# Optimization experiments

Measured on AMD Instinct MI355X. Metric: run time of the kernel, lower is better.

The kernel has to match this reference:

```python
import jax, jax.numpy as jnp
import numpy as np
import math

B, S, SIG, EMB, LAT, H, L_ENC, L_DEC = 16, 1024, 256, 256, 256, 8, 2, 2
EH, DH = EMB // H, LAT // H
EPS = 1e-10


def _sinusoidal_last_row(d):
    # last row of a standard sinusoidal PE table (position index = max_len-1)
    pos = 5000.0 - 1.0
    i = np.arange(d)
    angles = pos / np.power(10000.0, (2 * (i // 2)) / d)
    pe = np.where(i % 2 == 0, np.sin(angles), np.cos(angles))
    return jnp.asarray(pe, dtype=jnp.float32)


def setup_inputs() -> dict:
    key = jax.random.key(0)
    ks = iter(jax.random.split(key, 64))
    w = lambda *sh: 0.05 * jax.random.normal(next(ks), sh, dtype=jnp.float32)
    z = lambda *sh: jnp.zeros(sh, dtype=jnp.float32)
    d = {
        'inputData': jax.random.normal(next(ks), (B, S, SIG), dtype=jnp.float32),
        'pos_enc': _sinusoidal_last_row(SIG),
        'embW': w(SIG, EMB), 'embb': z(EMB),
        'qW': w(EMB, EMB), 'qb': z(EMB),
        'kW': w(EMB, EMB), 'kb': z(EMB),
        'vW': w(EMB, EMB), 'vb': z(EMB),
        'encBW': w(EH, EH), 'encBb': z(EH),
        'oW': w(EMB, EMB), 'ob': z(EMB),
        'ffe_W1': w(EMB, 2 * EMB), 'ffe_b1': z(2 * EMB),
        'ffe_W2': w(2 * EMB, EMB), 'ffe_b2': z(EMB),
        'lnSA_g': jnp.ones((L_ENC, EMB)), 'lnSA_b': z(L_ENC, EMB),
        'lnFF_g': jnp.ones((L_ENC, EMB)), 'lnFF_b': z(L_ENC, EMB),
        'start': w(1, LAT),
        'decQW': w(LAT, LAT), 'decQb': z(LAT),
        'decKW': w(EMB, EMB), 'decKb': z(EMB),
        'decVW': w(EMB, LAT), 'decVb': z(LAT),
        'decBW': w(EH + DH, DH), 'decBb': z(DH),
        'latW': w(LAT, LAT), 'latb': z(LAT),
        'ffd_W1': w(LAT, LAT // 2), 'ffd_b1': z(LAT // 2),
        'ffd_W2': w(LAT // 2, LAT), 'ffd_b2': z(LAT),
        'lnCA_g': jnp.ones((L_DEC, LAT)), 'lnCA_b': z(L_DEC, LAT),
        'lnLFF_g': jnp.ones((L_DEC, LAT)), 'lnLFF_b': z(L_DEC, LAT),
        'finW': w(LAT, LAT), 'finb': z(LAT),
    }
    return d


def _ln(x, g, b):
    m = x.mean(-1, keepdims=True)
    v = x.var(-1, keepdims=True)
    return (x - m) * jax.lax.rsqrt(v + EPS) * g + b


def _enc_attn(x, qW, qb, kW, kb, vW, vb, bW, bb, oW, ob):
    # x: (B,S,EMB) -> heads (B,H,S,EH)
    sp = lambda t: t.reshape(B, S, H, EH).transpose(0, 2, 1, 3)
    q, k, v = sp(x @ qW + qb), sp(x @ kW + kb), sp(x @ vW + vb)
    bk = k @ bW + bb                                   # bilinear key (B,H,S,EH)
    attn = jax.nn.softmax(jnp.einsum('bhqd,bhkd->bhqk', q, bk) / math.sqrt(EH), axis=-1)
    out = jnp.einsum('bhqk,bhkd->bhqd', attn, v)
    out = out.transpose(0, 2, 1, 3).reshape(B, S, EMB)
    return out @ oW + ob


def _dec_attn(enc, lat, qW, qb, kW, kb, vW, vb, bW, bb, oW, ob):
    # lat: (B,LAT) single query token; enc: (B,S,EMB)
    q = (lat @ qW + qb).reshape(B, 1, H, DH).transpose(0, 2, 1, 3)   # (B,H,1,DH)
    k = (enc @ kW + kb).reshape(B, S, H, EH).transpose(0, 2, 1, 3)   # (B,H,S,EH)
    v = (enc @ vW + vb).reshape(B, S, H, DH).transpose(0, 2, 1, 3)   # (B,H,S,DH)
    qcat = jnp.broadcast_to(q, (B, H, S, DH))
    kcat = jnp.concatenate([k, qcat], axis=-1)                       # (B,H,S,EH+DH)
    bk = kcat @ bW + bb                                              # (B,H,S,DH)
    attn = jax.nn.softmax(jnp.einsum('bhqd,bhkd->bhqk', q, bk) / math.sqrt(EH + DH), axis=-1)
    out = jnp.einsum('bhqk,bhkd->bhqd', attn, v)                     # (B,H,1,DH)
    out = out.transpose(0, 2, 1, 3).reshape(B, LAT)
    return out @ oW + ob


def reference(inputData, pos_enc, embW, embb, qW, qb, kW, kb, vW, vb, encBW, encBb,
              oW, ob, ffe_W1, ffe_b1, ffe_W2, ffe_b2, lnSA_g, lnSA_b, lnFF_g, lnFF_b,
              start, decQW, decQb, decKW, decKb, decVW, decVb, decBW, decBb,
              latW, latb, ffd_W1, ffd_b1, ffd_W2, ffd_b2, lnCA_g, lnCA_b,
              lnLFF_g, lnLFF_b, finW, finb):
    emb = (inputData + pos_enc) @ embW + embb          # (B,S,EMB)
    t = emb
    for l in range(L_ENC):
        n = _ln(t, lnSA_g[l], lnSA_b[l])
        a = _enc_attn(n, qW, qb, kW, kb, vW, vb, encBW, encBb, oW, ob) + n
        t = a + emb
        n2 = _ln(t, lnFF_g[l], lnFF_b[l])
        ff = jax.nn.selu(n2 @ ffe_W1 + ffe_b1) @ ffe_W2 + ffe_b2
        t = ff + n2
    init_lat = jnp.broadcast_to(start, (B, LAT))
    lat = init_lat
    for l in range(L_DEC):
        nl = _ln(init_lat, lnCA_g[l], lnCA_b[l])       # module always feeds initialLatentData
        lat = _dec_attn(t, nl, decQW, decQb, decKW, decKb, decVW, decVb,
                        decBW, decBb, latW, latb)
        nf = _ln(lat, lnLFF_g[l], lnLFF_b[l])
        lat = jax.nn.selu(nf @ ffd_W1 + ffd_b1) @ ffd_W2 + ffd_b2
    return lat @ finW + finb
```

## Files before the change

### kernel.cpp

```cpp
#include <hip/hip_runtime.h>
#include <hip/hip_bf16.h>
#include <math.h>

typedef __hip_bfloat16 bf16;

#define BB 16
#define SS 1024
#define NH 8
#define NR (BB*SS)
#define SZE ((size_t)NR*256)
#define RS 264

typedef __attribute__((ext_vector_type(8))) short short8;
typedef __attribute__((ext_vector_type(4))) float f32x4;
typedef __attribute__((ext_vector_type(8))) unsigned short u16x8;
typedef __attribute__((ext_vector_type(4))) unsigned short u16x4;

__device__ __forceinline__ float bf2f(bf16 x){ return __bfloat162float(x); }
__device__ __forceinline__ bf16  f2bf(float x){ return __float2bfloat16(x); }
__device__ __forceinline__ unsigned short f2bfu(float x){
  bf16 t = __float2bfloat16(x); return *reinterpret_cast<unsigned short*>(&t);
}
__device__ __forceinline__ float bfu2f(unsigned short u){
  return __uint_as_float(((unsigned)u)<<16);
}

__device__ __forceinline__ void stT(float* p, size_t i, float v){ p[i] = v; }
__device__ __forceinline__ void stT(bf16*  p, size_t i, float v){ p[i] = f2bf(v); }

__device__ __forceinline__ float selu_f(float x){
  const float a = 1.6732632423543772f, sc = 1.0507009873554805f;
  return sc * (x > 0.f ? x : a * expm1f(x));
}

__device__ __forceinline__ void gload16(const void* g, void* l){
  __builtin_amdgcn_global_load_lds(
      (const __attribute__((address_space(1))) unsigned int*)g,
      (__attribute__((address_space(3))) unsigned int*)l, 16, 0, 0);
}

struct PtrPack { const void* p[43]; };
struct TabPack { int off[43]; int cnt[43]; int total; };
struct TrTab   { int srcOff[12]; int K[12]; int N[12]; int dstOff[12]; int total; };

__global__ __launch_bounds__(256) void k_canon(PtrPack ptrs, TabPack tab,
    float* __restrict__ dst, int* __restrict__ flagw)
{
  unsigned w0 = ((const unsigned*)ptrs.p[18])[0];
  int isbf = (w0 == 0x3F803F80u) ? 1 : 0;
  if (blockIdx.x == 0 && threadIdx.x == 0) *flagw = isbf;
  __shared__ int so[43], sn[43];
  int tid = threadIdx.x;
  if (tid < 43){ so[tid] = tab.off[tid]; sn[tid] = tab.cnt[tid]; }
  __syncthreads();
  int g = blockIdx.x*256 + tid;
  if (g >= tab.total) return;
  int seg = 1;
  while (seg < 42 && g >= so[seg] + sn[seg]) seg++;
  int li = g - so[seg];
  float v = isbf ? bf2f(((const bf16*)ptrs.p[seg])[li])
                 : ((const float*)ptrs.p[seg])[li];
  dst[g] = v;
}

__global__ __launch_bounds__(256) void k_transW(const float* __restrict__ wt,
    TrTab tt, unsigned short* __restrict__ dst)
{
  int g = blockIdx.x*256 + threadIdx.x;
  if (g >= tt.total) return;
  int seg = 0;
  while (seg < 11 && g >= tt.dstOff[seg] + tt.K[seg]*tt.N[seg]) seg++;
  int li = g - tt.dstOff[seg];
  int K = tt.K[seg], N = tt.N[seg];
  int n = li / K, k = li - n*K;
  dst[g] = f2bfu(wt[tt.srcOff[seg] + (size_t)k*N + n]);
}

__global__ __launch_bounds__(256) void k_qfold(const float* __restrict__ wt,
    int qOff, int qbOff, int bwOff, unsigned short* __restrict__ qW2t,
    float* __restrict__ qbf)
{
  __shared__ float bw[32];
  int n = blockIdx.x, t = threadIdx.x;
  int h = n>>5, d = n&31;
  if (t < 32) bw[t] = wt[bwOff + d*32 + t];
  __syncthreads();
  float acc = 0.f;
  #pragma unroll 8
  for (int j = 0; j < 32; j++) acc += wt[qOff + (size_t)t*256 + h*32 + j]*bw[j];
  qW2t[(size_t)n*256 + t] = f2bfu(acc);
  if (t == 0){
    float a = 0.f;
    #pragma unroll 8
    for (int j = 0; j < 32; j++) a += wt[qbOff + h*32 + j]*bw[j];
    qbf[n] = a;
  }
}

template<int K, int LDA, int CT>
__device__ __forceinline__ void wave_gemmN(const unsigned short (*As)[LDA],
    const unsigned short* __restrict__ Wt, int n0, f32x4 acc[4][CT], int lane)
{
  int col = lane & 15, quad = lane >> 4;
  #pragma unroll
  for (int k0 = 0; k0 < K; k0 += 32){
    short8 a[4], b[CT];
    #pragma unroll
    for (int rt = 0; rt < 4; rt++)
      a[rt] = *(const short8*)(&As[rt*16 + col][k0 + quad*8]);
    #pragma unroll
    for (int ct = 0; ct < CT; ct++)
      b[ct] = *(const short8*)(&Wt[(size_t)(n0 + ct*16 + col)*K + k0 + quad*8]);
    #pragma unroll
    for (int rt = 0; rt < 4; rt++)
      #pragma unroll
      for (int ct = 0; ct < CT; ct++)
        acc[rt][ct] = __builtin_amdgcn_mfma_f32_16x16x32_bf16(a[rt], b[ct], acc[rt][ct], 0, 0, 0);
  }
}

template<int K, int LDA, int CT>
__device__ __forceinline__ void wave_gemmM32(const unsigned short (*As)[LDA],
    const unsigned short* __restrict__ Wt, int n0, f32x4 acc[2][CT], int lane)
{
  int col = lane & 15, quad = lane >> 4;
  #pragma unroll
  for (int k0 = 0; k0 < K; k0 += 32){
    short8 a[2], b[CT];
    #pragma unroll
    for (int rt = 0; rt < 2; rt++)
      a[rt] = *(const short8*)(&As[rt*16 + col][k0 + quad*8]);
    #pragma unroll
    for (int ct = 0; ct < CT; ct++)
      b[ct] = *(const short8*)(&Wt[(size_t)(n0 + ct*16 + col)*K + k0 + quad*8]);
    #pragma unroll
    for (int rt = 0; rt < 2; rt++)
      #pragma unroll
      for (int ct = 0; ct < CT; ct++)
        acc[rt][ct] = __builtin_amdgcn_mfma_f32_16x16x32_bf16(a[rt], b[ct], acc[rt][ct], 0, 0, 0);
  }
}

#define ZERO_ACC4(acc)  { _Pragma("unroll") for (int rt=0;rt<4;rt++){ _Pragma("unroll") for (int ct=0;ct<4;ct++) acc[rt][ct] = (f32x4){0.f,0.f,0.f,0.f}; } }
#define ZERO_ACC2(acc)  { _Pragma("unroll") for (int rt=0;rt<4;rt++){ _Pragma("unroll") for (int ct=0;ct<2;ct++) acc[rt][ct] = (f32x4){0.f,0.f,0.f,0.f}; } }
#define ZERO_ACC24(acc) { _Pragma("unroll") for (int rt=0;rt<2;rt++){ _Pragma("unroll") for (int ct=0;ct<4;ct++) acc[rt][ct] = (f32x4){0.f,0.f,0.f,0.f}; } }

#define EPI_BEGIN(e) { int rt = (e)>>4, ct = ((e)>>2)&3, r = (e)&3; \
    int lrow = rt*16 + quad*4 + r; int gcol0 = ct*16 + col; \
    float av = acc[rt][ct][r]; (void)lrow; (void)gcol0; (void)av;
#define EPI_END }

#define EPI32_BEGIN(e) { int rt = (e)>>4, ct = ((e)>>2)&3, r = (e)&3; \
    int lrow = rt*16 + quad*4 + r; int gcol0 = ct*16 + col; \
    float av = acc[rt][ct][r]; (void)lrow; (void)gcol0; (void)av;
#define EPI32_END }

template<int PRE, typename OT>
__global__ __launch_bounds__(256) void k_gemm_mfma(const void* __restrict__ A,
    const int* __restrict__ flagp, const float* __restrict__ pe,
    const unsigned short* __restrict__ Wt, const float* __restrict__ bias,
    OT* __restrict__ out)
{
  __shared__ __align__(16) unsigned short As[64][RS];
  int tid = threadIdx.x;
  int m = blockIdx.x & 255, nh = blockIdx.x >> 8;
  int row0 = m*64;
  if (PRE == 0){
    int f = *flagp;
    if (f){
      for (int jj = 0; jj < 8; jj++){
        int idx = tid + jj*256;
        int row = idx>>5, c8 = (idx&31)<<3;
        u16x8 xb = *(const u16x8*)((const unsigned short*)A
            + (size_t)(row0+row)*256 + c8);
        u16x8 o;
        #pragma unroll
        for (int i=0;i<8;i++) o[i] = f2bfu(bfu2f(xb[i]) + pe[c8+i]);
        *(u16x8*)(&As[row][c8]) = o;
      }
    } else {
      for (int jj = 0; jj < 16; jj++){
        int idx = tid + jj*256;
        int row = idx>>6, c4 = (idx&63)<<2;
        float4 x = *(const float4*)((const float*)A + (size_t)(row0+row)*256 + c4);
        u16x4 o;
        o[0] = f2bfu(x.x + pe[c4+0]);
        o[1] = f2bfu(x.y + pe[c4+1]);
        o[2] = f2bfu(x.z + pe[c4+2]);
        o[3] = f2bfu(x.w + pe[c4+3]);
        *(u16x4*)(&As[row][c4]) = o;
      }
    }
  } else {
    for (int jj = 0; jj < 16; jj++){
      int idx = tid + jj*256;
      int row = idx>>6, c4 = (idx&63)<<2;
      float4 x = *(const float4*)((const float*)A + (size_t)(row0+row)*256 + c4);
      *(u16x4*)(&As[row][c4]) = (u16x4){f2bfu(x.x),f2bfu(x.y),f2bfu(x.z),f2bfu(x.w)};
    }
  }
  __syncthreads();
  int w = tid>>6, lane = tid&63, col = lane&15, quad = lane>>4;
  int n0 = nh*128 + w*32;
  f32x4 acc[4][2];
  ZERO_ACC2(acc);
  wave_gemmN<256, RS, 2>(As, Wt, n0, acc, lane);
  #pragma unroll
  for (int rt = 0; rt < 4; rt++){
    #pragma unroll
    for (int ct = 0; ct < 2; ct++){
      #pragma unroll
      for (int r = 0; r < 4; r++){
        int grow = row0 + rt*16 + quad*4 + r;
        int gcol = n0 + ct*16 + col;
        stT(out, (size_t)grow*256 + gcol, acc[rt][ct][r] + bias[gcol]);
      }
    }
  }
}

__global__ __launch_bounds__(256) void k_decKV(const float* __restrict__ A,
    const unsigned short* __restrict__ KWt, const float* __restrict__ kb,
    const unsigned short* __restrict__ VWt, const float* __restrict__ vb,
    bf16* __restrict__ ko, bf16* __restrict__ vo)
{
  __shared__ __align__(16) unsigned short As[64][RS];
  int tid = threadIdx.x;
  int m = blockIdx.x & 255, nh = blockIdx.x >> 8;
  int row0 = m*64;
  for (int jj = 0; jj < 16; jj++){
    int idx = tid + jj*256;
    int row = idx>>6, c4 = (idx&63)<<2;
    float4 x = *(const float4*)(A + (size_t)(row0+row)*256 + c4);
    *(u16x4*)(&As[row][c4]) = (u16x4){f2bfu(x.x),f2bfu(x.y),f2bfu(x.z),f2bfu(x.w)};
  }
  __syncthreads();
  int w = tid>>6, lane = tid&63, col = lane&15, quad = lane>>4;
  int n0 = nh*128 + w*32;
  f32x4 acc[4][2];
  ZERO_ACC2(acc);
  wave_gemmN<256, RS, 2>(As, KWt, n0, acc, lane);
  #pragma unroll
  for (int rt = 0; rt < 4; rt++){
    #pragma unroll
    for (int ct = 0; ct < 2; ct++){
      #pragma unroll
      for (int r = 0; r < 4; r++){
        int grow = row0 + rt*16 + quad*4 + r;
        int gcol = n0 + ct*16 + col;
        ko[(size_t)grow*256 + gcol] = f2bf(acc[rt][ct][r] + kb[gcol]);
      }
    }
  }
  ZERO_ACC2(acc);
  wave_gemmN<256, RS, 2>(As, VWt, n0, acc, lane);
  #pragma unroll
  for (int rt = 0; rt < 4; rt++){
    #pragma unroll
    for (int ct = 0; ct < 2; ct++){
      #pragma unroll
      for (int r = 0; r < 4; r++){
        int grow = row0 + rt*16 + quad*4 + r;
        int gcol = n0 + ct*16 + col;
        vo[(size_t)grow*256 + gcol] = f2bf(acc[rt][ct][r] + vb[gcol]);
      }
    }
  }
}

__global__ __launch_bounds__(256) void k_qkvbk_mfma(const float* __restrict__ tsrc,
    const float* __restrict__ lng, const float* __restrict__ lnb,
    const unsigned short* __restrict__ qW2t, const float* __restrict__ qbf,
    const unsigned short* __restrict__ kWt, const float* __restrict__ kb,
    const unsigned short* __restrict__ vWt, const float* __restrict__ vb,
    bf16* __restrict__ qo, bf16* __restrict__ vo, bf16* __restrict__ bko)
{
  __shared__ __align__(16) unsigned short Ns[64][RS];
  __shared__ float mArr[64], rArr[64];
  int tid = threadIdx.x;
  int m = blockIdx.x & 255, nh = blockIdx.x >> 8;
  int row0 = m*64;
  int b = row0 >> 10, s0 = row0 & 1023;
  {
    int row = tid>>2, l4 = tid&3;
    const float4* rp = (const float4*)(tsrc + (size_t)(row0+row)*256) + l4*16;
    float s = 0.f, s2 = 0.f;
    #pragma unroll 4
    for (int c = 0; c < 16; c++){
      float4 x = rp[c];
      s += x.x + x.y + x.z + x.w;
      s2 += x.x*x.x + x.y*x.y + x.z*x.z + x.w*x.w;
    }
    s  += __shfl_down(s, 2, 4);  s  += __shfl_down(s, 1, 4);
    s2 += __shfl_down(s2, 2, 4); s2 += __shfl_down(s2, 1, 4);
    if (l4 == 0){
      float mn = s*(1.f/256.f);
      float v = s2*(1.f/256.f) - mn*mn;
      mArr[row] = mn; rArr[row] = rsqrtf(fmaxf(v,0.f) + 1e-10f);
    }
  }
  __syncthreads();
  for (int jj = 0; jj < 16; jj++){
    int idx = tid + jj*256;
    int row = idx>>6, c4 = (idx&63)<<2;
    float4 x = *(const float4*)(tsrc + (size_t)(row0+row)*256 + c4);
    float mn = mArr[row], rr = rArr[row];
    u16x4 o;
    o[0] = f2bfu((x.x - mn)*rr*lng[c4+0] + lnb[c4+0]);
    o[1] = f2bfu((x.y - mn)*rr*lng[c4+1] + lnb[c4+1]);
    o[2] = f2bfu((x.z - mn)*rr*lng[c4+2] + lnb[c4+2]);
    o[3] = f2bfu((x.w - mn)*rr*lng[c4+3] + lnb[c4+3]);
    *(u16x4*)(&Ns[row][c4]) = o;
  }
  __syncthreads();
  int w = tid>>6, lane = tid&63, col = lane&15, quad = lane>>4;
  int n0 = nh*128 + w*32;
  f32x4 acc[4][2];
  ZERO_ACC2(acc);
  wave_gemmN<256, RS, 2>(Ns, qW2t, n0, acc, lane);
  #pragma unroll
  for (int rt = 0; rt < 4; rt++){
    #pragma unroll
    for (int ct = 0; ct < 2; ct++){
      #pragma unroll
      for (int r = 0; r < 4; r++){
        int grow = row0 + rt*16 + quad*4 + r;
        int gcol = n0 + ct*16 + col;
        qo[(size_t)grow*256 + gcol] = f2bf(acc[rt][ct][r] + qbf[gcol]);
      }
    }
  }
  ZERO_ACC2(acc);
  wave_gemmN<256, RS, 2>(Ns, vWt, n0, acc, lane);
  #pragma unroll
  for (int rt = 0; rt < 4; rt++){
    #pragma unroll
    for (int ct = 0; ct < 2; ct++){
      #pragma unroll
      for (int r = 0; r < 4; r++){
        int grow = row0 + rt*16 + quad*4 + r;
        int gcol = n0 + ct*16 + col;
        vo[(size_t)grow*256 + gcol] = f2bf(acc[rt][ct][r] + vb[gcol]);
      }
    }
  }
  ZERO_ACC2(acc);
  wave_gemmN<256, RS, 2>(Ns, kWt, n0, acc, lane);
  int h = nh*4 + w;
  #pragma unroll
  for (int rt = 0; rt < 4; rt++){
    #pragma unroll
    for (int ct = 0; ct < 2; ct++){
      #pragma unroll
      for (int r = 0; r < 4; r++){
        int srow = s0 + rt*16 + quad*4 + r;
        int d = ct*16 + col;
        bko[(((size_t)(b*NH+h))*SS + srow)*32 + d] =
            f2bf(acc[rt][ct][r] + kb[h*32 + d]);
      }
    }
  }
}

__global__ __launch_bounds__(256) void k_attn_mfma(
    const bf16* __restrict__ q, const bf16* __restrict__ bk,
    const bf16* __restrict__ v, bf16* __restrict__ ao)
{
  int bi = blockIdx.x;
  int qq = bi >> 7, b = (bi >> 3) & 15, h = bi & 7;
  int tid = threadIdx.x;
  int w = tid>>6, lane = tid&63;
  int quad = lane>>4, col = lane&15;
  int q0 = qq*128 + w*32;

  __shared__ __align__(16) unsigned short Ks2b[2][64][32];
  __shared__ __align__(16) unsigned short Vt2b[2][32][76];

  const float scale2 = 0.17677669529663687f * 1.4426950408889634f;
  short8 aq[2];
  #pragma unroll
  for (int rt = 0; rt < 2; rt++){
    const unsigned short* gq = (const unsigned short*)q
        + ((size_t)(b*SS + q0 + rt*16 + col))*256 + h*32 + quad*8;
    u16x8 qv = *(const u16x8*)gq;
    #pragma unroll
    for (int i=0;i<8;i++) aq[rt][i] = (short)f2bfu(bfu2f(qv[i])*scale2);
  }

  float l_r[2] = {0.f, 0.f};
  f32x4 o[2][2];
  #pragma unroll
  for (int rt=0;rt<2;rt++)
    #pragma unroll
    for (int ct=0;ct<2;ct++) o[rt][ct] = (f32x4){0.f,0.f,0.f,0.f};

  int krow = tid>>2, ksl = tid&3;
  int kslw = ksl ^ ((krow>>1)&3);
  int vk0 = tid>>3, vdg = tid&7;
  int vk1 = vk0 + 32;
  int rsl = (quad ^ ((col>>1)&3))*8;

  const unsigned short* bkp = (const unsigned short*)bk + ((size_t)(b*NH+h))*SS*32;
  const unsigned short* vp  = (const unsigned short*)v + (size_t)b*SS*256 + h*32;

  u16x8 rK;
  u16x4 rV0, rV1;
  rK  = *(const u16x8*)(bkp + (size_t)krow*32 + ksl*8);
  rV0 = *(const u16x4*)(vp + (size_t)vk0*256 + vdg*4);
  rV1 = *(const u16x4*)(vp + (size_t)vk1*256 + vdg*4);

  for (int kt = 0; kt < 16; kt++){
    int cb = kt & 1;
    *(u16x8*)(&Ks2b[cb][krow][kslw*8]) = rK;
    #pragma unroll
    for (int i=0;i<4;i++) Vt2b[cb][vdg*4+i][vk0] = rV0[i];
    #pragma unroll
    for (int i=0;i<4;i++) Vt2b[cb][vdg*4+i][vk1] = rV1[i];
    __syncthreads();
    if (kt < 15){
      int nk = kt + 1;
      rK  = *(const u16x8*)(bkp + (size_t)(nk*64 + krow)*32 + ksl*8);
      rV0 = *(const u16x4*)(vp + (size_t)(nk*64 + vk0)*256 + vdg*4);
      rV1 = *(const u16x4*)(vp + (size_t)(nk*64 + vk1)*256 + vdg*4);
    }
    #pragma unroll
    for (int g = 0; g < 2; g++){
      unsigned pk[2][4];
      #pragma unroll
      for (int tt = 0; tt < 2; tt++){
        int t4 = g*2 + tt;
        short8 bk8 = *(const short8*)(&Ks2b[cb][t4*16 + col][rsl]);
        #pragma unroll
        for (int rt = 0; rt < 2; rt++){
          f32x4 s = __builtin_amdgcn_mfma_f32_16x16x32_bf16(bk8, aq[rt],
                      (f32x4){0.f,0.f,0.f,0.f}, 0, 0, 0);
          float e0 = __builtin_amdgcn_exp2f(s[0]);
          float e1 = __builtin_amdgcn_exp2f(s[1]);
          float e2 = __builtin_amdgcn_exp2f(s[2]);
          float e3 = __builtin_amdgcn_exp2f(s[3]);
          l_r[rt] += (e0+e1)+(e2+e3);
          pk[rt][tt*2+0] = __builtin_amdgcn_perm(
              __float_as_uint(e1), __float_as_uint(e0), 0x07060302u);
          pk[rt][tt*2+1] = __builtin_amdgcn_perm(
              __float_as_uint(e3), __float_as_uint(e2), 0x07060302u);
        }
      }
      short8 av[2];
      #pragma unroll
      for (int ct = 0; ct < 2; ct++){
        u16x4 v0 = *(const u16x4*)(&Vt2b[cb][ct*16+col][(g*2+0)*16 + quad*4]);
        u16x4 v1 = *(const u16x4*)(&Vt2b[cb][ct*16+col][(g*2+1)*16 + quad*4]);
        av[ct][0]=(short)v0[0]; av[ct][1]=(short)v0[1];
        av[ct][2]=(short)v0[2]; av[ct][3]=(short)v0[3];
        av[ct][4]=(short)v1[0]; av[ct][5]=(short)v1[1];
        av[ct][6]=(short)v1[2]; av[ct][7]=(short)v1[3];
      }
      #pragma unroll
      for (int rt = 0; rt < 2; rt++){
        union { unsigned u[4]; short8 s8; } pb;
        pb.u[0]=pk[rt][0]; pb.u[1]=pk[rt][1]; pb.u[2]=pk[rt][2]; pb.u[3]=pk[rt][3];
        #pragma unroll
        for (int ct = 0; ct < 2; ct++)
          o[rt][ct] = __builtin_amdgcn_mfma_f32_16x16x32_bf16(
              av[ct], pb.s8, o[rt][ct], 0, 0, 0);
      }
    }
  }
  #pragma unroll
  for (int rt=0;rt<2;rt++){
    float l = l_r[rt];
    l += __shfl_xor(l, 16, 64);
    l += __shfl_xor(l, 32, 64);
    float inv = 1.f / l;
    size_t obase = ((size_t)(b*SS + q0 + rt*16 + col))*256 + h*32;
    #pragma unroll
    for (int ct=0;ct<2;ct++){
      u16x4 ov;
      #pragma unroll
      for (int r=0;r<4;r++) ov[r] = f2bfu(o[rt][ct][r]*inv);
      *(u16x4*)((unsigned short*)ao + obase + ct*16 + quad*4) = ov;
    }
  }
}

__global__ __launch_bounds__(256) void k_oln_mfma(
    const float* __restrict__ tsrc, const float* __restrict__ emb,
    const bf16* __restrict__ ao,
    const float* __restrict__ lnSAg, const float* __restrict__ lnSAb,
    const unsigned short* __restrict__ oWt, const float* __restrict__ ob,
    const float* __restrict__ lnFFg, const float* __restrict__ lnFFb,
    bf16* __restrict__ n2o)
{
  __shared__ __align__(16) unsigned short Aos[32][RS];
  __shared__ __align__(16) unsigned short Tm[32][RS];
  __shared__ float mArr[32], rArr[32];
  int tid = threadIdx.x, row0 = blockIdx.x*32;
  {
    int row = tid>>3, l8 = tid&7;
    const float4* rp = (const float4*)(tsrc + (size_t)(row0+row)*256) + l8*8;
    float s = 0.f, s2 = 0.f;
    #pragma unroll
    for (int c = 0; c < 8; c++){
      float4 x = rp[c];
      s += x.x + x.y + x.z + x.w;
      s2 += x.x*x.x + x.y*x.y + x.z*x.z + x.w*x.w;
    }
    s  += __shfl_down(s, 4, 8);  s  += __shfl_down(s, 2, 8);  s  += __shfl_down(s, 1, 8);
    s2 += __shfl_down(s2, 4, 8); s2 += __shfl_down(s2, 2, 8); s2 += __shfl_down(s2, 1, 8);
    if (l8 == 0){
      float m = s*(1.f/256.f);
      float v = s2*(1.f/256.f) - m*m;
      mArr[row] = m; rArr[row] = rsqrtf(fmaxf(v,0.f) + 1e-10f);
    }
  }
  for (int jj = 0; jj < 4; jj++){
    int idx = tid + jj*256;
    int row = idx>>5, c8 = idx&31;
    *(u16x8*)(&Aos[row][c8*8]) =
        *(const u16x8*)((const unsigned short*)ao + (size_t)(row0+row)*256 + c8*8);
  }
  __syncthreads();
  int w = tid>>6, lane = tid&63, col = lane&15, quad = lane>>4;
  f32x4 acc[2][4];
  ZERO_ACC24(acc);
  wave_gemmM32<256, RS, 4>(Aos, oWt, w*64, acc, lane);
  #pragma unroll
  for (int e = 0; e < 32; e++){
    EPI32_BEGIN(e)
    int gcol = w*64 + gcol0;
    size_t g = (size_t)(row0+lrow)*256 + gcol;
    float n1 = (tsrc[g] - mArr[lrow])*rArr[lrow]*lnSAg[gcol] + lnSAb[gcol];
    Tm[lrow][gcol] = f2bfu(av + ob[gcol] + n1 + emb[g]);
    EPI32_END
  }
  __syncthreads();
  {
    int row = tid>>3, l8 = tid&7;
    float s = 0.f, s2 = 0.f;
    for (int c = l8; c < 256; c += 8){ float x = bfu2f(Tm[row][c]); s += x; s2 += x*x; }
    s  += __shfl_down(s, 4, 8);  s  += __shfl_down(s, 2, 8);  s  += __shfl_down(s, 1, 8);
    s2 += __shfl_down(s2, 4, 8); s2 += __shfl_down(s2, 2, 8); s2 += __shfl_down(s2, 1, 8);
    if (l8 == 0){
      float m = s*(1.f/256.f);
      float v = s2*(1.f/256.f) - m*m;
      mArr[row] = m; rArr[row] = rsqrtf(fmaxf(v,0.f) + 1e-10f);
    }
  }
  __syncthreads();
  for (int jj = 0; jj < 8; jj++){
    int idx = tid + jj*256;
    int row = idx>>6, c4 = (idx&63)<<2;
    float mn = mArr[row], rr = rArr[row];
    u16x4 tv = *(const u16x4*)(&Tm[row][c4]);
    u16x4 ov;
    ov[0] = f2bfu((bfu2f(tv[0]) - mn)*rr*lnFFg[c4+0] + lnFFb[c4+0]);
    ov[1] = f2bfu((bfu2f(tv[1]) - mn)*rr*lnFFg[c4+1] + lnFFb[c4+1]);
    ov[2] = f2bfu((bfu2f(tv[2]) - mn)*rr*lnFFg[c4+2] + lnFFb[c4+2]);
    ov[3] = f2bfu((bfu2f(tv[3]) - mn)*rr*lnFFg[c4+3] + lnFFb[c4+3]);
    *(u16x4*)((unsigned short*)n2o + (size_t)(row0+row)*256 + c4) = ov;
  }
}

#define FF_STAGE(B, KT) { \
  int k0 = (KT)*64; \
  _Pragma("unroll") \
  for (int i = 0; i < 4; i++){ int c = w*4 + i; \
    gload16(A  + (size_t)(row0 + c*8 + rsub)*KFULL + k0 + sgo, &As[B][c*512]); } \
  _Pragma("unroll") \
  for (int i = 0; i < 2; i++){ int c = w*2 + i; \
    gload16(Wb + (size_t)(n0   + c*8 + rsub)*KFULL + k0 + sgo, &Bs[B][c*512]); } }

#define FF_COMPUTE(B) { \
  _Pragma("unroll") \
  for (int kk = 0; kk < 2; kk++){ \
    short8 a[4], b2r[2]; \
    _Pragma("unroll") \
    for (int rt = 0; rt < 4; rt++) \
      a[rt] = *(const short8*)(&As[B][((wr*64 + rt*16 + col)<<6) + ((((kk<<2)|quad) ^ (col&7))<<3)]); \
    _Pragma("unroll") \
    for (int ct = 0; ct < 2; ct++) \
      b2r[ct] = *(const short8*)(&Bs[B][((wc*32 + ct*16 + col)<<6) + ((((kk<<2)|quad) ^ (col&7))<<3)]); \
    _Pragma("unroll") \
    for (int rt = 0; rt < 4; rt++) \
      _Pragma("unroll") \
      for (int ct = 0; ct < 2; ct++) \
        acc[rt][ct] = __builtin_amdgcn_mfma_f32_16x16x32_bf16(a[rt], b2r[ct], acc[rt][ct], 0, 0, 0); } }

template<int KFULL, int NFULL, int EPI>
__global__ __launch_bounds__(256) void k_ff_gemm(const bf16* __restrict__ A,
    const unsigned short* __restrict__ Wt, const float* __restrict__ bias,
    const bf16* __restrict__ res, void* __restrict__ outv)
{
  __shared__ __align__(16) unsigned short As[2][128*64];
  __shared__ __align__(16) unsigned short Bs[2][64*64];
  constexpr int NWG = 128 * (NFULL/64);
  constexpr int NKT = KFULL/64;
  int tid = threadIdx.x;
  int w = tid>>6, lane = tid&63;
  int col = lane&15, quad = lane>>4;
  int wr = w>>1, wc = w&1;
  int rsub = lane>>3;
  int sgo = (((lane&7) ^ rsub)<<3);
  int bid = blockIdx.x;
  int swz = (bid & 7)*(NWG>>3) + (bid >> 3);
  int mb = swz & 127, nb = swz >> 7;
  int row0 = mb*128, n0 = nb*64;
  const bf16* Wb = (const bf16*)Wt;

  f32x4 acc[4][2];
  ZERO_ACC2(acc);

  FF_STAGE(0, 0);
  __syncthreads();
  #pragma unroll
  for (int kt = 0; kt < NKT-1; kt++){
    int cb = kt & 1;
    FF_STAGE(cb^1, kt+1);
    FF_COMPUTE(cb);
    __syncthreads();
  }
  FF_COMPUTE((NKT-1)&1);

  if (EPI == 0){
    bf16* o = (bf16*)outv;
    #pragma unroll
    for (int rt = 0; rt < 4; rt++){
      #pragma unroll
      for (int ct = 0; ct < 2; ct++){
        #pragma unroll
        for (int r = 0; r < 4; r++){
          int grow = row0 + wr*64 + rt*16 + quad*4 + r;
          int gcol = n0 + wc*32 + ct*16 + col;
          o[(size_t)grow*NFULL + gcol] = f2bf(selu_f(acc[rt][ct][r] + bias[gcol]));
        }
      }
    }
  } else {
    float* o = (float*)outv;
    #pragma unroll
    for (int rt = 0; rt < 4; rt++){
      #pragma unroll
      for (int ct = 0; ct < 2; ct++){
        #pragma unroll
        for (int r = 0; r < 4; r++){
          int grow = row0 + wr*64 + rt*16 + quad*4 + r;
          int gcol = n0 + wc*32 + ct*16 + col;
          size_t g = (size_t)grow*NFULL + gcol;
          o[g] = acc[rt][ct][r] + bias[gcol] + bf2f(res[g]);
        }
      }
    }
  }
}

__global__ __launch_bounds__(256) void k_dec_head(const float* __restrict__ startp,
    const float* __restrict__ lng, const float* __restrict__ lnb,
    const float* __restrict__ decQW, const float* __restrict__ decQb,
    const float* __restrict__ decBW,
    float* __restrict__ s_q, float* __restrict__ s_qc)
{
  __shared__ float s1[256], s2[256], nl[256], qv[256];
  int t = threadIdx.x;
  float v = startp[t];
  s1[t]=v; s2[t]=v*v; __syncthreads();
  for (int s=128;s>0;s>>=1){
    if (t<s){ s1[t]+=s1[t+s]; s2[t]+=s2[t+s]; }
    __syncthreads();
  }
  float m = s1[0]*(1.f/256.f);
  float var = s2[0]*(1.f/256.f) - m*m;
  float r = rsqrtf(fmaxf(var,0.f) + 1e-10f);
  nl[t] = (v-m)*r*lng[t] + lnb[t];
  __syncthreads();
  float acc = decQb[t];
  for (int k=0;k<256;k++) acc += nl[k]*decQW[k*256+t];
  qv[t] = acc; s_q[t] = acc;
  __syncthreads();
  int h = t>>5, d = t&31;
  float a = 0.f;
  #pragma unroll 8
  for (int e=0;e<32;e++) a += qv[h*32+e]*decBW[(32+e)*32 + d];
  s_qc[t] = a;
}

__global__ __launch_bounds__(256) void k_bkdec_mfma(const bf16* __restrict__ kk,
    const float* __restrict__ qc, const unsigned short* __restrict__ decBWt,
    const float* __restrict__ Bb, bf16* __restrict__ bko)
{
  __shared__ __align__(16) unsigned short Ks[64][RS];
  int tid = threadIdx.x, row0 = blockIdx.x*64;
  int b = row0 >> 10, s0 = row0 & 1023;
  for (int jj = 0; jj < 8; jj++){
    int idx = tid + jj*256;
    int row = idx>>5, c8 = idx&31;
    *(u16x8*)(&Ks[row][c8*8]) =
        *(const u16x8*)((const unsigned short*)kk + (size_t)(row0+row)*256 + c8*8);
  }
  __syncthreads();
  int w = tid>>6, lane = tid&63, col = lane&15, quad = lane>>4;
  f32x4 acc[4][4];
  ZERO_ACC4(acc);
  #pragma unroll
  for (int ct = 0; ct < 4; ct++){
    int base = w*64 + ct*16;
    int h = base >> 5, d0 = base & 31;
    short8 bfrag = *(const short8*)(&decBWt[(size_t)(d0 + col)*32 + quad*8]);
    #pragma unroll
    for (int rt = 0; rt < 4; rt++){
      short8 afrag = *(const short8*)(&Ks[rt*16 + col][h*32 + quad*8]);
      acc[rt][ct] = __builtin_amdgcn_mfma_f32_16x16x32_bf16(afrag, bfrag, acc[rt][ct], 0, 0, 0);
    }
  }
  #pragma unroll
  for (int e = 0; e < 64; e++){
    EPI_BEGIN(e)
    int srow = s0 + lrow;
    int gcol = w*64 + gcol0;
    int h = gcol >> 5, d = gcol & 31;
    bko[(((size_t)(b*NH+h))*SS + srow)*32 + d] = f2bf(av + qc[gcol] + Bb[d]);
    EPI_END
  }
}

__global__ __launch_bounds__(256) void k_attn_dec(const float* __restrict__ q,
    const bf16* __restrict__ bk, const bf16* __restrict__ v,
    float* __restrict__ out)
{
  int h = blockIdx.x & 7, b = blockIdx.x >> 3;
  int tid = threadIdx.x;
  __shared__ float qs[32];
  __shared__ float sc[SS];
  __shared__ float red[256];
  if (tid < 32) qs[tid] = q[h*32 + tid] * (0.125f * 1.4426950408889634f);
  __syncthreads();
  float lsum = 0.f;
  for (int jj=0;jj<4;jj++){
    int j = tid*4 + jj;
    size_t base = (((size_t)(b*NH+h))*SS + j)*32;
    float s = 0.f;
    #pragma unroll
    for (int d=0;d<32;d++) s += qs[d]*bf2f(bk[base + d]);
    float e = __builtin_amdgcn_exp2f(s);
    sc[j] = e; lsum += e;
  }
  red[tid] = lsum; __syncthreads();
  for (int s=128;s>0;s>>=1){ if (tid<s) red[tid]+=red[tid+s]; __syncthreads(); }
  float gs = red[0];
  __syncthreads();
  int d = tid & 31, c = tid >> 5;
  float acc = 0.f;
  for (int j=c*128; j<c*128+128; j++)
    acc += sc[j]*bf2f(v[((size_t)(b*SS + j))*256 + h*32 + d]);
  red[c*32+d] = acc;
  __syncthreads();
  if (tid < 32){
    float s = 0.f;
    #pragma unroll
    for (int cc=0;cc<8;cc++) s += red[cc*32+tid];
    out[b*256 + h*32 + tid] = s / gs;
  }
}

__global__ __launch_bounds__(256) void k_dec_tail(const float* __restrict__ s_ao,
    const float* __restrict__ latW, const float* __restrict__ latb,
    const float* __restrict__ lng, const float* __restrict__ lnb,
    const float* __restrict__ W1, const float* __restrict__ b1,
    const float* __restrict__ W2, const float* __restrict__ b2,
    const float* __restrict__ finW, const float* __restrict__ finb,
    const int* __restrict__ flagp, void* __restrict__ outv)
{
  __shared__ float x[256], y[256], s1[256], s2[256];
  int t = threadIdx.x, b = blockIdx.x;
  x[t] = s_ao[b*256 + t];
  __syncthreads();
  float lat = latb[t];
  for (int k=0;k<256;k++) lat += x[k]*latW[k*256+t];
  s1[t]=lat; s2[t]=lat*lat; __syncthreads();
  for (int s=128;s>0;s>>=1){
    if (t<s){ s1[t]+=s1[t+s]; s2[t]+=s2[t+s]; }
    __syncthreads();
  }
  float m = s1[0]*(1.f/256.f);
  float var = s2[0]*(1.f/256.f) - m*m;
  float r = rsqrtf(fmaxf(var,0.f) + 1e-10f);
  y[t] = (lat-m)*r*lng[t] + lnb[t];
  __syncthreads();
  if (t < 128){
    float a2 = b1[t];
    for (int k=0;k<256;k++) a2 += y[k]*W1[k*128+t];
    x[t] = selu_f(a2);
  }
  __syncthreads();
  float a3 = b2[t];
  for (int k=0;k<128;k++) a3 += x[k]*W2[k*256+t];
  s1[t] = a3;
  __syncthreads();
  float o = finb[t];
  for (int k=0;k<256;k++) o += s1[k]*finW[k*256+t];
  size_t oi = (size_t)b*256 + t;
  if (*flagp) ((bf16*)outv)[oi] = f2bf(o);
  else        ((float*)outv)[oi] = o;
}

extern "C" void kernel_launch(void* const* d_in, const int* in_sizes, int n_in,
                              void* d_out, int out_size, void* d_ws, size_t ws_size,
                              hipStream_t stream)
{
  static const int cnts[43] = {
    0,256,65536,256,65536,256,65536,256,65536,256,1024,32,65536,256,
    131072,512,131072,256,512,512,512,512,256,65536,256,65536,256,65536,256,
    2048,32,65536,256,32768,128,32768,256,512,512,512,512,65536,256 };
  TabPack tab; int acc0 = 0;
  for (int i = 0; i < 43; i++){ tab.off[i] = acc0; tab.cnt[i] = cnts[i]; acc0 += cnts[i]; }
  tab.total = acc0;
  PtrPack ptrs;
  for (int i = 0; i < 43; i++) ptrs.p[i] = d_in[i];

  char* p = (char*)d_ws;
  float* wt   = (float*)p;
  int*  flagp = (int*)(p + (4u<<20));
  char* bigc  = p + (4u<<20) + 256;
  float* g_emb = (float*)bigc;
  float* g_t   = (float*)(bigc + SZE*4);
  bf16*  g_q   = (bf16*)(bigc + 2*SZE*4);
  bf16*  g_v   = (bf16*)(bigc + 2*SZE*4 + SZE*2);
  bf16*  g_ao  = (bf16*)(bigc + 2*SZE*4 + 2*SZE*2);
  bf16*  g_bk  = (bf16*)(bigc + 2*SZE*4 + 3*SZE*2);
  float* fsm   = (float*)(bigc + 2*SZE*4 + 4*SZE*2);
  unsigned short* wtr = (unsigned short*)(bigc + 2*SZE*4 + 4*SZE*2 + 131072*4);
  float* s_q  = fsm;
  float* s_qc = fsm + 256;
  float* s_ao = fsm + 512;
  float* qbf  = fsm + 8192;
  bf16*  g_h1 = g_v;

  static const int trIdx[10] = {2,4,6,8,12,14,16,25,27,10};
  static const int trK[10]   = {256,256,256,256,256,256,512,256,256,32};
  static const int trN[10]   = {256,256,256,256,256,512,256,256,256,32};
  TrTab tr; int tacc = 0;
  for (int i = 0; i < 10; i++){
    tr.srcOff[i] = tab.off[trIdx[i]];
    tr.K[i] = trK[i]; tr.N[i] = trN[i];
    tr.dstOff[i] = tacc; tacc += trK[i]*trN[i];
  }
  tr.srcOff[10] = tab.off[29];        tr.K[10]=32; tr.N[10]=32; tr.dstOff[10]=tacc; tacc+=1024;
  tr.srcOff[11] = tab.off[29] + 1024; tr.K[11]=32; tr.N[11]=32; tr.dstOff[11]=tacc; tacc+=1024;
  tr.total = tacc;
  const unsigned short *embWt = wtr + tr.dstOff[0],
    *kWt = wtr + tr.dstOff[2], *vWt = wtr + tr.dstOff[3], *oWt = wtr + tr.dstOff[4],
    *ffeW1t = wtr + tr.dstOff[5], *ffeW2t = wtr + tr.dstOff[6],
    *decKWt = wtr + tr.dstOff[7], *decVWt = wtr + tr.dstOff[8],
    *decBWtk = wtr + tr.dstOff[10];
  unsigned short* qW2t = wtr + tr.total;

  #define WP(i) (wt + tab.off[i])
  const float *pe=WP(1), *embb=WP(3), *qb=WP(5), *kb=WP(7), *vb=WP(9),
    *ob=WP(13), *ffeb1=WP(15), *ffeb2=WP(17),
    *lnSAg=WP(18), *lnSAb=WP(19), *lnFFg=WP(20), *lnFFb=WP(21),
    *startp=WP(22), *decQW=WP(23), *decQb=WP(24), *decKb=WP(26),
    *decVb=WP(28), *decBW=WP(29), *decBb=WP(30), *latW=WP(31),
    *latb=WP(32), *ffdW1=WP(33), *ffdb1=WP(34), *ffdW2=WP(35), *ffdb2=WP(36),
    *lnCAg=WP(37), *lnCAb=WP(38), *lnLFFg=WP(39), *lnLFFb=WP(40),
    *finW=WP(41), *finb=WP(42);

  dim3 blk(256);
  const int G64  = NR/64;
  const int G32  = NR/32;
  const int GSP  = 512;
  const int GA2  = 1024;
  const int LD   = 1;

  k_canon<<<(tab.total+255)/256, blk, 0, stream>>>(ptrs, tab, wt, flagp);
  k_transW<<<(tr.total+255)/256, blk, 0, stream>>>(wt, tr, wtr);
  k_qfold<<<256, blk, 0, stream>>>(wt, tab.off[4], tab.off[5], tab.off[10], qW2t, qbf);

  k_gemm_mfma<0,float><<<GSP, blk, 0, stream>>>(d_in[0], flagp, pe, embWt, embb, g_emb);

  const float* tcur = g_emb;
  for (int l = 0; l < 2; l++){
    k_qkvbk_mfma<<<GSP, blk, 0, stream>>>(tcur, lnSAg+l*256, lnSAb+l*256,
        qW2t, qbf, kWt, kb, vWt, vb, g_q, g_v, g_bk);
    k_attn_mfma<<<GA2, blk, 0, stream>>>(g_q, g_bk, g_v, g_ao);
    k_oln_mfma<<<G32, blk, 0, stream>>>(tcur, g_emb, g_ao,
        lnSAg+l*256, lnSAb+l*256, oWt, ob, lnFFg+l*256, lnFFb+l*256, g_q);
    k_ff_gemm<256,512,0><<<1024, blk, 0, stream>>>(g_q, ffeW1t, ffeb1, (const bf16*)nullptr, g_h1);
    k_ff_gemm<512,256,1><<<512, blk, 0, stream>>>(g_h1, ffeW2t, ffeb2, g_q, g_t);
    tcur = g_t;
  }

  k_dec_head<<<1, blk, 0, stream>>>(startp, lnCAg+LD*256, lnCAb+LD*256,
      decQW, decQb, decBW, s_q, s_qc);
  k_decKV<<<GSP, blk, 0, stream>>>(g_t, decKWt, decKb, decVWt, decVb, g_q, g_v);
  k_bkdec_mfma<<<G64, blk, 0, stream>>>(g_q, s_qc, decBWtk, decBb, g_bk);
  k_attn_dec<<<BB*NH, blk, 0, stream>>>(s_q, g_bk, g_v, s_ao);
  k_dec_tail<<<BB, blk, 0, stream>>>(s_ao, latW, latb, lnLFFg+LD*256, lnLFFb+LD*256,
      ffdW1, ffdb1, ffdW2, ffdb2, finW, finb, flagp, d_out);
  #undef WP
}
```

Baseline: 478.1 us.

## Double-buffer weight tiles in LDS for QKV and decoder KV GEMMs

Replaces the direct global-memory weight reads in wave_gemmN with a double-buffered LDS staging scheme for k_qkvbk_mfma and k_decKV. Each 64-wide K slice of the weight is loaded asynchronously with gload16 into a swizzled shared buffer while MFMAs run on the previous slice, and the next matrix's first slice is prefetched during the current epilogue. This is meant to hide global load latency and share weight loads across the waves of a block. In exchange it uses about 32KB more LDS per block, which may lower occupancy, and adds extra block-wide barriers.

```diff
diff --git a/kernel.cpp b/kernel.cpp
--- a/kernel.cpp
+++ b/kernel.cpp
@@ -219,52 +219,85 @@
   }
 }
 
+#define QKV_STAGE(B, WPTR, KT) { \
+  _Pragma("unroll") \
+  for (int i = 0; i < 4; i++){ int c = w*4 + i; \
+    gload16(WPTR + (size_t)(nh*128 + c*8 + rsub)*256 + (KT)*64 + sgo, &Bs[B][c*512]); } }
+
+#define QKV_COMPUTE(B, KT) { \
+  _Pragma("unroll") \
+  for (int kk = 0; kk < 2; kk++){ \
+    short8 a[4], b2[2]; \
+    _Pragma("unroll") \
+    for (int rt = 0; rt < 4; rt++) \
+      a[rt] = *(const short8*)(&Ns[rt*16 + col][(KT)*64 + kk*32 + quad*8]); \
+    _Pragma("unroll") \
+    for (int ct = 0; ct < 2; ct++) \
+      b2[ct] = *(const short8*)(&Bs[B][((w*32 + ct*16 + col)<<6) + ((((kk<<2)|quad) ^ (col&7))<<3)]); \
+    _Pragma("unroll") \
+    for (int rt = 0; rt < 4; rt++) \
+      _Pragma("unroll") \
+      for (int ct = 0; ct < 2; ct++) \
+        acc[rt][ct] = __builtin_amdgcn_mfma_f32_16x16x32_bf16(a[rt], b2[ct], acc[rt][ct], 0, 0, 0); } }
+
 __global__ __launch_bounds__(256) void k_decKV(const float* __restrict__ A,
     const unsigned short* __restrict__ KWt, const float* __restrict__ kb,
     const unsigned short* __restrict__ VWt, const float* __restrict__ vb,
     bf16* __restrict__ ko, bf16* __restrict__ vo)
 {
-  __shared__ __align__(16) unsigned short As[64][RS];
+  __shared__ __align__(16) unsigned short Ns[64][RS];
+  __shared__ __align__(16) unsigned short Bs[2][128*64];
   int tid = threadIdx.x;
   int m = blockIdx.x & 255, nh = blockIdx.x >> 8;
   int row0 = m*64;
+  int w = tid>>6, lane = tid&63, col = lane&15, quad = lane>>4;
+  int rsub = lane>>3;
+  int sgo = (((lane&7) ^ rsub)<<3);
   for (int jj = 0; jj < 16; jj++){
     int idx = tid + jj*256;
     int row = idx>>6, c4 = (idx&63)<<2;
     float4 x = *(const float4*)(A + (size_t)(row0+row)*256 + c4);
-    *(u16x4*)(&As[row][c4]) = (u16x4){f2bfu(x.x),f2bfu(x.y),f2bfu(x.z),f2bfu(x.w)};
-  }
-  __syncthreads();
-  int w = tid>>6, lane = tid&63, col = lane&15, quad = lane>>4;
-  int n0 = nh*128 + w*32;
+    *(u16x4*)(&Ns[row][c4]) = (u16x4){f2bfu(x.x),f2bfu(x.y),f2bfu(x.z),f2bfu(x.w)};
+  }
+  QKV_STAGE(0, KWt, 0);
+  __syncthreads();
   f32x4 acc[4][2];
   ZERO_ACC2(acc);
-  wave_gemmN<256, RS, 2>(As, KWt, n0, acc, lane);
-  #pragma unroll
-  for (int rt = 0; rt < 4; rt++){
-    #pragma unroll
-    for (int ct = 0; ct < 2; ct++){
-      #pragma unroll
-      for (int r = 0; r < 4; r++){
-        int grow = row0 + rt*16 + quad*4 + r;
-        int gcol = n0 + ct*16 + col;
-        ko[(size_t)grow*256 + gcol] = f2bf(acc[rt][ct][r] + kb[gcol]);
-      }
-    }
+  QKV_STAGE(1, KWt, 1); QKV_COMPUTE(0, 0); __syncthreads();
+  QKV_STAGE(0, KWt, 2); QKV_COMPUTE(1, 1); __syncthreads();
+  QKV_STAGE(1, KWt, 3); QKV_COMPUTE(0, 2); __syncthreads();
+  QKV_STAGE(0, VWt, 0); QKV_COMPUTE(1, 3);
+  {
+    int n0 = nh*128 + w*32;
+    #pragma unroll
+    for (int rt = 0; rt < 4; rt++)
+      #pragma unroll
+      for (int ct = 0; ct < 2; ct++)
+        #pragma unroll
+        for (int r = 0; r < 4; r++){
+          int grow = row0 + rt*16 + quad*4 + r;
+          int gcol = n0 + ct*16 + col;
+          ko[(size_t)grow*256 + gcol] = f2bf(acc[rt][ct][r] + kb[gcol]);
+        }
   }
   ZERO_ACC2(acc);
-  wave_gemmN<256, RS, 2>(As, VWt, n0, acc, lane);
-  #pragma unroll
-  for (int rt = 0; rt < 4; rt++){
-    #pragma unroll
-    for (int ct = 0; ct < 2; ct++){
-      #pragma unroll
-      for (int r = 0; r < 4; r++){
-        int grow = row0 + rt*16 + quad*4 + r;
-        int gcol = n0 + ct*16 + col;
-        vo[(size_t)grow*256 + gcol] = f2bf(acc[rt][ct][r] + vb[gcol]);
-      }
-    }
+  __syncthreads();
+  QKV_STAGE(1, VWt, 1); QKV_COMPUTE(0, 0); __syncthreads();
+  QKV_STAGE(0, VWt, 2); QKV_COMPUTE(1, 1); __syncthreads();
+  QKV_STAGE(1, VWt, 3); QKV_COMPUTE(0, 2); __syncthreads();
+  QKV_COMPUTE(1, 3);
+  {
+    int n0 = nh*128 + w*32;
+    #pragma unroll
+    for (int rt = 0; rt < 4; rt++)
+      #pragma unroll
+      for (int ct = 0; ct < 2; ct++)
+        #pragma unroll
+        for (int r = 0; r < 4; r++){
+          int grow = row0 + rt*16 + quad*4 + r;
+          int gcol = n0 + ct*16 + col;
+          vo[(size_t)grow*256 + gcol] = f2bf(acc[rt][ct][r] + vb[gcol]);
+        }
   }
 }
 
@@ -276,11 +309,15 @@
     bf16* __restrict__ qo, bf16* __restrict__ vo, bf16* __restrict__ bko)
 {
   __shared__ __align__(16) unsigned short Ns[64][RS];
+  __shared__ __align__(16) unsigned short Bs[2][128*64];
   __shared__ float mArr[64], rArr[64];
   int tid = threadIdx.x;
   int m = blockIdx.x & 255, nh = blockIdx.x >> 8;
   int row0 = m*64;
   int b = row0 >> 10, s0 = row0 & 1023;
+  int w = tid>>6, lane = tid&63, col = lane&15, quad = lane>>4;
+  int rsub = lane>>3;
+  int sgo = (((lane&7) ^ rsub)<<3);
   {
     int row = tid>>2, l4 = tid&3;
     const float4* rp = (const float4*)(tsrc + (size_t)(row0+row)*256) + l4*16;
@@ -312,53 +349,65 @@
     o[3] = f2bfu((x.w - mn)*rr*lng[c4+3] + lnb[c4+3]);
     *(u16x4*)(&Ns[row][c4]) = o;
   }
-  __syncthreads();
-  int w = tid>>6, lane = tid&63, col = lane&15, quad = lane>>4;
-  int n0 = nh*128 + w*32;
+  QKV_STAGE(0, qW2t, 0);
+  __syncthreads();
   f32x4 acc[4][2];
   ZERO_ACC2(acc);
-  wave_gemmN<256, RS, 2>(Ns, qW2t, n0, acc, lane);
-  #pragma unroll
-  for (int rt = 0; rt < 4; rt++){
-    #pragma unroll
-    for (int ct = 0; ct < 2; ct++){
-      #pragma unroll
-      for (int r = 0; r < 4; r++){
-        int grow = row0 + rt*16 + quad*4 + r;
-        int gcol = n0 + ct*16 + col;
-        qo[(size_t)grow*256 + gcol] = f2bf(acc[rt][ct][r] + qbf[gcol]);
-      }
-    }
+  QKV_STAGE(1, qW2t, 1); QKV_COMPUTE(0, 0); __syncthreads();
+  QKV_STAGE(0, qW2t, 2); QKV_COMPUTE(1, 1); __syncthreads();
+  QKV_STAGE(1, qW2t, 3); QKV_COMPUTE(0, 2); __syncthreads();
+  QKV_STAGE(0, vWt,  0); QKV_COMPUTE(1, 3);
+  {
+    int n0 = nh*128 + w*32;
+    #pragma unroll
+    for (int rt = 0; rt < 4; rt++)
+      #pragma unroll
+      for (int ct = 0; ct < 2; ct++)
+        #pragma unroll
+        for (int r = 0; r < 4; r++){
+          int grow = row0 + rt*16 + quad*4 + r;
+          int gcol = n0 + ct*16 + col;
+          qo[(size_t)grow*256 + gcol] = f2bf(acc[rt][ct][r] + qbf[gcol]);
+        }
   }
   ZERO_ACC2(acc);
-  wave_gemmN<256, RS, 2>(Ns, vWt, n0, acc, lane);
-  #pragma unroll
-  for (int rt = 0; rt < 4; rt++){
-    #pragma unroll
-    for (int ct = 0; ct < 2; ct++){
-      #pragma unroll
-      for (int r = 0; r < 4; r++){
-        int grow = row0 + rt*16 + quad*4 + r;
-        int gcol = n0 + ct*16 + col;
-        vo[(size_t)grow*256 + gcol] = f2bf(acc[rt][ct][r] + vb[gcol]);
-      }
-    }
+  __syncthreads();
+  QKV_STAGE(1, vWt, 1); QKV_COMPUTE(0, 0); __syncthreads();
+  QKV_STAGE(0, vWt, 2); QKV_COMPUTE(1, 1); __syncthreads();
+  QKV_STAGE(1, vWt, 3); QKV_COMPUTE(0, 2); __syncthreads();
+  QKV_STAGE(0, kWt, 0); QKV_COMPUTE(1, 3);
+  {
+    int n0 = nh*128 + w*32;
+    #pragma unroll
+    for (int rt = 0; rt < 4; rt++)
+      #pragma unroll
+      for (int ct = 0; ct < 2; ct++)
+        #pragma unroll
+        for (int r = 0; r < 4; r++){
+          int grow = row0 + rt*16 + quad*4 + r;
+          int gcol = n0 + ct*16 + col;
+          vo[(size_t)grow*256 + gcol] = f2bf(acc[rt][ct][r] + vb[gcol]);
+        }
   }
   ZERO_ACC2(acc);
-  wave_gemmN<256, RS, 2>(Ns, kWt, n0, acc, lane);
-  int h = nh*4 + w;
-  #pragma unroll
-  for (int rt = 0; rt < 4; rt++){
-    #pragma unroll
-    for (int ct = 0; ct < 2; ct++){
-      #pragma unroll
-      for (int r = 0; r < 4; r++){
-        int srow = s0 + rt*16 + quad*4 + r;
-        int d = ct*16 + col;
-        bko[(((size_t)(b*NH+h))*SS + srow)*32 + d] =
-            f2bf(acc[rt][ct][r] + kb[h*32 + d]);
-      }
-    }
+  __syncthreads();
+  QKV_STAGE(1, kWt, 1); QKV_COMPUTE(0, 0); __syncthreads();
+  QKV_STAGE(0, kWt, 2); QKV_COMPUTE(1, 1); __syncthreads();
+  QKV_STAGE(1, kWt, 3); QKV_COMPUTE(0, 2); __syncthreads();
+  QKV_COMPUTE(1, 3);
+  {
+    int h = nh*4 + w;
+    #pragma unroll
+    for (int rt = 0; rt < 4; rt++)
+      #pragma unroll
+      for (int ct = 0; ct < 2; ct++)
+        #pragma unroll
+        for (int r = 0; r < 4; r++){
+          int srow = s0 + rt*16 + quad*4 + r;
+          int d = ct*16 + col;
+          bko[(((size_t)(b*NH+h))*SS + srow)*32 + d] =
+              f2bf(acc[rt][ct][r] + kb[h*32 + d]);
+        }
   }
 }
 
```

Result: faster. 468.3 us (median of 2 runs) (-2.0%).
